# Performance work log

Hardware: AMD Instinct MI355X
Metric: run time of the kernel (lower is better)

The kernel has to match this reference:

```python
import jax, jax.numpy as jnp
import numpy as np

N = 100000       # nodes
E = 3200000      # edges (avg degree 32)
C_IN = 32        # input_channels


def _glorot(key, shape):
    lim = float(np.sqrt(6.0 / (shape[0] + shape[1])))
    return jax.random.uniform(key, shape, jnp.float32, -lim, lim)


def setup_inputs() -> dict:
    key = jax.random.key(0)
    ks = jax.random.split(key, 8)
    x = jax.random.normal(ks[0], (N, C_IN), jnp.float32)
    edge_index = jax.random.randint(ks[1], (2, E), 0, N, dtype=jnp.int64)
    return {
        "x": x,
        "edge_index": edge_index,
        "W1": _glorot(ks[2], (C_IN, 16)), "b1": jnp.zeros((16,), jnp.float32),
        "W2": _glorot(ks[3], (16, 32)),   "b2": jnp.zeros((32,), jnp.float32),
        "W3": _glorot(ks[4], (32, 16)),   "b3": jnp.zeros((16,), jnp.float32),
        "Wfc": _glorot(ks[5], (16, 1)),   "bfc": jnp.zeros((1,), jnp.float32),
    }


def _gcn_conv(x, W, b, src, dst, norm, n):
    # PyG GCNConv: transform then degree-normalized scatter-add (self-loops in src/dst)
    h = x @ W                              # [N, out]
    m = h[src] * norm[:, None]             # gather + per-edge scale
    return jax.ops.segment_sum(m, dst, num_segments=n) + b


def reference(x, edge_index, W1, b1, W2, b2, W3, b3, Wfc, bfc):
    n = x.shape[0]
    loops = jnp.arange(n, dtype=edge_index.dtype)
    src = jnp.concatenate([edge_index[0], loops])   # add self-loops
    dst = jnp.concatenate([edge_index[1], loops])
    deg = jax.ops.segment_sum(jnp.ones(src.shape[0], x.dtype), dst, num_segments=n)
    dis = jnp.where(deg > 0, jax.lax.rsqrt(deg), jnp.zeros((), x.dtype))
    norm = dis[src] * dis[dst]                      # symmetric D^-1/2 A D^-1/2

    h = jax.nn.relu(_gcn_conv(x, W1, b1, src, dst, norm, n))
    h = jax.nn.relu(_gcn_conv(h, W2, b2, src, dst, norm, n))
    h = jax.nn.relu(_gcn_conv(h, W3, b3, src, dst, norm, n))
    out = h @ Wfc + bfc                             # [N, 1]
    return jnp.mean(out)
```

## Files before the change

kernel.cpp:

```cpp
#include <hip/hip_runtime.h>

static constexpr int BLK = 256;
static constexpr int CHUNK = 4096;
static constexpr int BSHIFT = 7;
static constexpr int BNODES = 128;
static constexpr int MAXNB = 1024;

__device__ __forceinline__ float bf_lo(unsigned u) { return __uint_as_float(u << 16); }
__device__ __forceinline__ float bf_hi(unsigned u) { return __uint_as_float(u & 0xFFFF0000u); }
__device__ __forceinline__ unsigned bf_r(float f) {
    unsigned x = __float_as_uint(f);
    x += 0x7fffu + ((x >> 16) & 1u);
    return x >> 16;
}
__device__ __forceinline__ unsigned bf_pack(float lo, float hi) {
    return bf_r(lo) | (bf_r(hi) << 16);
}


__global__ __launch_bounds__(BLK) void k_hist(const int* __restrict__ dst, int* __restrict__ ghist,
                                              int e, int NB, int NBLK) {
    __shared__ int h[MAXNB];
    for (int i = threadIdx.x; i < NB; i += BLK) h[i] = 0;
    __syncthreads();
    int base = blockIdx.x * CHUNK;
    int lim = min(e - base, CHUNK);
    bool v4 = ((((size_t)(dst + base)) & 15) == 0);
    if (v4 && lim == CHUNK) {
        const int4* d4 = (const int4*)(dst + base);
        for (int q = threadIdx.x; q < CHUNK / 4; q += BLK) {
            int4 v = d4[q];
            atomicAdd(&h[v.x >> BSHIFT], 1);
            atomicAdd(&h[v.y >> BSHIFT], 1);
            atomicAdd(&h[v.z >> BSHIFT], 1);
            atomicAdd(&h[v.w >> BSHIFT], 1);
        }
    } else {
        for (int r = threadIdx.x; r < lim; r += BLK) atomicAdd(&h[dst[base + r] >> BSHIFT], 1);
    }
    __syncthreads();
    for (int b = threadIdx.x; b < NB; b += BLK) ghist[b * NBLK + blockIdx.x] = h[b];
}

__global__ void k_scan1(const int* __restrict__ in, int* __restrict__ excl,
                        int* __restrict__ partials, int n) {
    __shared__ int s[BLK];
    int i = blockIdx.x * BLK + threadIdx.x;
    int v = (i < n) ? in[i] : 0;
    s[threadIdx.x] = v;
    __syncthreads();
    for (int off = 1; off < BLK; off <<= 1) {
        int t = ((int)threadIdx.x >= off) ? s[threadIdx.x - off] : 0;
        __syncthreads();
        s[threadIdx.x] += t;
        __syncthreads();
    }
    if (i < n) excl[i] = s[threadIdx.x] - v;
    if (threadIdx.x == BLK - 1) partials[blockIdx.x] = s[BLK - 1];
}

__global__ void k_scan2(int* __restrict__ partials, int P) {
    __shared__ int s[1024];
    int carry = 0;
    for (int base = 0; base < P; base += 1024) {
        int i = base + (int)threadIdx.x;
        int v = (i < P) ? partials[i] : 0;
        s[threadIdx.x] = v;
        __syncthreads();
        for (int off = 1; off < 1024; off <<= 1) {
            int t = ((int)threadIdx.x >= off) ? s[threadIdx.x - off] : 0;
            __syncthreads();
            s[threadIdx.x] += t;
            __syncthreads();
        }
        if (i < P) partials[i] = carry + s[threadIdx.x] - v;
        carry += s[1023];
        __syncthreads();
    }
}

__global__ void k_scan3(int* __restrict__ excl, const int* __restrict__ partials, int n) {
    int i = blockIdx.x * BLK + threadIdx.x;
    if (i < n) excl[i] += partials[blockIdx.x];
}

__global__ __launch_bounds__(BLK) void k_bin(const int* __restrict__ src, const int* __restrict__ dst,
                                             const int* __restrict__ goff, unsigned int* __restrict__ keys,
                                             int e, int NB, int NBLK) {
    __shared__ int hcur[MAXNB];
    __shared__ int sstart[MAXNB + 1];
    __shared__ unsigned int stage[CHUNK];
    __shared__ unsigned short bkt[CHUNK];
    for (int i = threadIdx.x; i < NB; i += BLK) hcur[i] = 0;
    __syncthreads();
    int base = blockIdx.x * CHUNK;
    int lim = min(e - base, CHUNK);
    bool v4 = ((((size_t)(dst + base)) & 15) == 0) && ((((size_t)(src + base)) & 15) == 0) && (lim == CHUNK);
    if (v4) {
        const int4* d4 = (const int4*)(dst + base);
        for (int q = threadIdx.x; q < CHUNK / 4; q += BLK) {
            int4 v = d4[q];
            atomicAdd(&hcur[v.x >> BSHIFT], 1);
            atomicAdd(&hcur[v.y >> BSHIFT], 1);
            atomicAdd(&hcur[v.z >> BSHIFT], 1);
            atomicAdd(&hcur[v.w >> BSHIFT], 1);
        }
    } else {
        for (int r = threadIdx.x; r < lim; r += BLK) atomicAdd(&hcur[dst[base + r] >> BSHIFT], 1);
    }
    __syncthreads();
    for (int i = threadIdx.x; i < MAXNB; i += BLK) sstart[i] = (i < NB) ? hcur[i] : 0;
    __syncthreads();
    for (int off = 1; off < MAXNB; off <<= 1) {
        int tv[MAXNB / BLK];
#pragma unroll
        for (int j = 0; j < MAXNB / BLK; ++j) {
            int i = (int)threadIdx.x + j * BLK;
            tv[j] = (i >= off) ? sstart[i - off] : 0;
        }
        __syncthreads();
#pragma unroll
        for (int j = 0; j < MAXNB / BLK; ++j) sstart[(int)threadIdx.x + j * BLK] += tv[j];
        __syncthreads();
    }
    int ex[MAXNB / BLK];
#pragma unroll
    for (int j = 0; j < MAXNB / BLK; ++j) {
        int i = (int)threadIdx.x + j * BLK;
        ex[j] = sstart[i] - ((i < NB) ? hcur[i] : 0);
    }
    __syncthreads();
#pragma unroll
    for (int j = 0; j < MAXNB / BLK; ++j) {
        int i = (int)threadIdx.x + j * BLK;
        sstart[i] = ex[j];
        if (i < NB) hcur[i] = ex[j];
    }
    __syncthreads();
    if (v4) {
        const int4* s4 = (const int4*)(src + base);
        const int4* d4 = (const int4*)(dst + base);
        for (int q = threadIdx.x; q < CHUNK / 4; q += BLK) {
            int4 sv = s4[q];
            int4 dv = d4[q];
#pragma unroll
            for (int u = 0; u < 4; ++u) {
                int s = (u == 0) ? sv.x : (u == 1) ? sv.y : (u == 2) ? sv.z : sv.w;
                int d = (u == 0) ? dv.x : (u == 1) ? dv.y : (u == 2) ? dv.z : dv.w;
                int b = d >> BSHIFT;
                int pos = atomicAdd(&hcur[b], 1);
                stage[pos] = (unsigned)s | ((unsigned)(d & (BNODES - 1)) << 20);
                bkt[pos] = (unsigned short)b;
            }
        }
    } else {
        for (int r = threadIdx.x; r < lim; r += BLK) {
            int s = src[base + r], d = dst[base + r];
            int b = d >> BSHIFT;
            int pos = atomicAdd(&hcur[b], 1);
            stage[pos] = (unsigned)s | ((unsigned)(d & (BNODES - 1)) << 20);
            bkt[pos] = (unsigned short)b;
        }
    }
    __syncthreads();
    for (int j = threadIdx.x; j < lim; j += BLK) {
        int b = bkt[j];
        keys[goff[b * NBLK + blockIdx.x] + (j - sstart[b])] = stage[j];
    }
}

__global__ __launch_bounds__(BLK) void k_sortb(const unsigned int* __restrict__ keys,
                                               const int* __restrict__ goff,
                                               unsigned int* __restrict__ sorted,
                                               int* __restrict__ node_off, float* __restrict__ dis,
                                               int n, int NB, int NBLK, int e) {
    __shared__ int cnt[BNODES];
    __shared__ int sc[BNODES];
    __shared__ int cur[BNODES];
    int b = blockIdx.x;
    int start = goff[b * NBLK];
    int end = (b + 1 < NB) ? goff[(b + 1) * NBLK] : e;
    if (threadIdx.x < BNODES) cnt[threadIdx.x] = 0;
    __syncthreads();
    int astart = (start + 3) & ~3;
    if (astart > end) astart = end;
    int nq = (end - astart) >> 2;
    for (int k = start + (int)threadIdx.x; k < astart; k += BLK) atomicAdd(&cnt[keys[k] >> 20], 1);
    {
        const uint4* k4 = (const uint4*)(keys + astart);
        for (int q = threadIdx.x; q < nq; q += BLK) {
            uint4 v = k4[q];
            atomicAdd(&cnt[v.x >> 20], 1);
            atomicAdd(&cnt[v.y >> 20], 1);
            atomicAdd(&cnt[v.z >> 20], 1);
            atomicAdd(&cnt[v.w >> 20], 1);
        }
    }
    for (int k = astart + (nq << 2) + (int)threadIdx.x; k < end; k += BLK) atomicAdd(&cnt[keys[k] >> 20], 1);
    __syncthreads();
    if (threadIdx.x < BNODES) sc[threadIdx.x] = cnt[threadIdx.x];
    __syncthreads();
    for (int off = 1; off < BNODES; off <<= 1) {
        int v = ((int)threadIdx.x < BNODES && (int)threadIdx.x >= off) ? sc[threadIdx.x - off] : 0;
        __syncthreads();
        if ((int)threadIdx.x < BNODES) sc[threadIdx.x] += v;
        __syncthreads();
    }
    if ((int)threadIdx.x < BNODES) {
        int excl = sc[threadIdx.x] - cnt[threadIdx.x];
        cur[threadIdx.x] = start + excl;
        int d = b * BNODES + (int)threadIdx.x;
        if (d < n) {
            node_off[d] = start + excl;
            dis[d] = rsqrtf(1.0f + (float)cnt[threadIdx.x]);
        }
    }
    if (b == NB - 1 && threadIdx.x == 0) node_off[n] = e;
    __syncthreads();
    for (int k = start + (int)threadIdx.x; k < astart; k += BLK) {
        unsigned key = keys[k];
        int pos = atomicAdd(&cur[key >> 20], 1);
        sorted[pos] = key & 0xFFFFFu;
    }
    {
        const uint4* k4 = (const uint4*)(keys + astart);
        for (int q = threadIdx.x; q < nq; q += BLK) {
            uint4 v = k4[q];
#pragma unroll
            for (int u = 0; u < 4; ++u) {
                unsigned key = (u == 0) ? v.x : (u == 1) ? v.y : (u == 2) ? v.z : v.w;
                int pos = atomicAdd(&cur[key >> 20], 1);
                sorted[pos] = key & 0xFFFFFu;
            }
        }
    }
    for (int k = astart + (nq << 2) + (int)threadIdx.x; k < end; k += BLK) {
        unsigned key = keys[k];
        int pos = atomicAdd(&cur[key >> 20], 1);
        sorted[pos] = key & 0xFFFFFu;
    }
}


template <int CIN, int COUT, bool BIAS, bool RELU_OUT, bool SCALE_OUT>
__global__ void k_transform(const float* __restrict__ in, const float* __restrict__ W,
                            const float* __restrict__ bias, const float* __restrict__ dis,
                            float* __restrict__ out, int n) {
    int t = blockIdx.x * BLK + threadIdx.x;
    int node = t / COUT, c = t % COUT;
    if (node >= n) return;
    const float* row = in + (size_t)node * CIN;
    float acc = BIAS ? bias[c] : 0.0f;
#pragma unroll
    for (int k = 0; k < CIN; ++k) acc = fmaf(row[k], W[k * COUT + c], acc);
    if (RELU_OUT) acc = fmaxf(acc, 0.0f);
    if (SCALE_OUT) acc *= dis[node];
    out[t] = acc;
}

__global__ void k_transform1_bf(const float* __restrict__ in, const float* __restrict__ W,
                                const float* __restrict__ dis, unsigned* __restrict__ out, int n) {
    int t = blockIdx.x * BLK + threadIdx.x;
    int node = t >> 3, j = t & 7;
    if (node >= n) return;
    const float* row = in + (size_t)node * 32;
    float a0 = 0.0f, a1 = 0.0f;
#pragma unroll
    for (int k = 0; k < 32; ++k) {
        float v = row[k];
        a0 = fmaf(v, W[k * 16 + 2 * j], a0);
        a1 = fmaf(v, W[k * 16 + 2 * j + 1], a1);
    }
    float sd = dis[node];
    out[t] = bf_pack(a0 * sd, a1 * sd);
}

template <int WMODE>
__global__ __launch_bounds__(BLK) void k_agg(const unsigned* __restrict__ in, const float* __restrict__ dis,
                                             const float* __restrict__ bias,
                                             const float* __restrict__ W2, const float* __restrict__ b2,
                                             const float* __restrict__ W3,
                                             const float* __restrict__ Wfc, const float* __restrict__ bfc,
                                             const unsigned int* __restrict__ sorted,
                                             const int* __restrict__ node_off,
                                             void* __restrict__ outv, int n) {
    int t = blockIdx.x * BLK + threadIdx.x;
    int d = t >> 2, j = t & 3;
    bool valid = d < n;
    int dd = valid ? d : 0;
    int k = node_off[dd], end = node_off[dd + 1];
    if (!valid) end = k;
    const uint2* inrow = (const uint2*)in;
    uint2 zz; zz.x = 0u; zz.y = 0u;
    uint2 ws = valid ? inrow[((size_t)dd << 2) + j] : zz;
    float a00 = bf_lo(ws.x), a10 = bf_hi(ws.x), a20 = bf_lo(ws.y), a30 = bf_hi(ws.y);
    float a01 = 0.0f, a11 = 0.0f, a21 = 0.0f, a31 = 0.0f;
    for (; k < end && (k & 3); ++k) {
        uint2 w = inrow[((size_t)sorted[k] << 2) + j];
        a00 += bf_lo(w.x); a10 += bf_hi(w.x); a20 += bf_lo(w.y); a30 += bf_hi(w.y);
    }
    for (; k + 7 < end; k += 8) {
        uint4 i0 = *(const uint4*)(sorted + k);
        uint4 i1 = *(const uint4*)(sorted + k + 4);
        uint2 w0 = inrow[((size_t)i0.x << 2) + j];
        uint2 w1 = inrow[((size_t)i0.y << 2) + j];
        uint2 w2 = inrow[((size_t)i0.z << 2) + j];
        uint2 w3 = inrow[((size_t)i0.w << 2) + j];
        uint2 w4 = inrow[((size_t)i1.x << 2) + j];
        uint2 w5 = inrow[((size_t)i1.y << 2) + j];
        uint2 w6 = inrow[((size_t)i1.z << 2) + j];
        uint2 w7 = inrow[((size_t)i1.w << 2) + j];
        a00 += (bf_lo(w0.x) + bf_lo(w2.x)) + (bf_lo(w4.x) + bf_lo(w6.x));
        a01 += (bf_lo(w1.x) + bf_lo(w3.x)) + (bf_lo(w5.x) + bf_lo(w7.x));
        a10 += (bf_hi(w0.x) + bf_hi(w2.x)) + (bf_hi(w4.x) + bf_hi(w6.x));
        a11 += (bf_hi(w1.x) + bf_hi(w3.x)) + (bf_hi(w5.x) + bf_hi(w7.x));
        a20 += (bf_lo(w0.y) + bf_lo(w2.y)) + (bf_lo(w4.y) + bf_lo(w6.y));
        a21 += (bf_lo(w1.y) + bf_lo(w3.y)) + (bf_lo(w5.y) + bf_lo(w7.y));
        a30 += (bf_hi(w0.y) + bf_hi(w2.y)) + (bf_hi(w4.y) + bf_hi(w6.y));
        a31 += (bf_hi(w1.y) + bf_hi(w3.y)) + (bf_hi(w5.y) + bf_hi(w7.y));
    }
    for (; k < end; ++k) {
        uint2 w = inrow[((size_t)sorted[k] << 2) + j];
        a00 += bf_lo(w.x); a10 += bf_hi(w.x); a20 += bf_lo(w.y); a30 += bf_hi(w.y);
    }
    float sd = dis[dd];
    float a0 = (a00 + a01) * sd;
    float a1 = (a10 + a11) * sd;
    float a2 = (a20 + a21) * sd;
    float a3 = (a30 + a31) * sd;

    if (WMODE == 0) {
        uint2* out = (uint2*)outv;
        if (valid) {
            uint2 r;
            r.x = bf_pack(sd * fmaxf(bias[4 * j] + a0, 0.0f), sd * fmaxf(bias[4 * j + 1] + a1, 0.0f));
            r.y = bf_pack(sd * fmaxf(bias[4 * j + 2] + a2, 0.0f), sd * fmaxf(bias[4 * j + 3] + a3, 0.0f));
            out[((size_t)d << 2) + j] = r;
        }
    } else if (WMODE == 1) {
        float hh[8];
#pragma unroll
        for (int p = 0; p < 8; ++p) hh[p] = b2[j + 4 * p];
#pragma unroll
        for (int kk = 0; kk < 4; ++kk) {
            float r0 = __shfl(a0, kk, 4);
            float r1 = __shfl(a1, kk, 4);
            float r2 = __shfl(a2, kk, 4);
            float r3 = __shfl(a3, kk, 4);
#pragma unroll
            for (int p = 0; p < 8; ++p) {
                int m = j + 4 * p;
                hh[p] = fmaf(r0, W2[(4 * kk) * 32 + m], hh[p]);
                hh[p] = fmaf(r1, W2[(4 * kk + 1) * 32 + m], hh[p]);
                hh[p] = fmaf(r2, W2[(4 * kk + 2) * 32 + m], hh[p]);
                hh[p] = fmaf(r3, W2[(4 * kk + 3) * 32 + m], hh[p]);
            }
        }
#pragma unroll
        for (int p = 0; p < 8; ++p) hh[p] = fmaxf(hh[p], 0.0f);
        float z0 = 0.0f, z1 = 0.0f, z2 = 0.0f, z3 = 0.0f;
#pragma unroll
        for (int kk = 0; kk < 4; ++kk) {
#pragma unroll
            for (int p = 0; p < 8; ++p) {
                float u = __shfl(hh[p], kk, 4);
                int m = kk + 4 * p;
                z0 = fmaf(u, W3[m * 16 + 4 * j], z0);
                z1 = fmaf(u, W3[m * 16 + 4 * j + 1], z1);
                z2 = fmaf(u, W3[m * 16 + 4 * j + 2], z2);
                z3 = fmaf(u, W3[m * 16 + 4 * j + 3], z3);
            }
        }
        uint2* out = (uint2*)outv;
        if (valid) {
            uint2 r;
            r.x = bf_pack(z0 * sd, z1 * sd);
            r.y = bf_pack(z2 * sd, z3 * sd);
            out[((size_t)d << 2) + j] = r;
        }
    } else {
        float* partials = (float*)outv;
        float contrib = 0.0f;
        if (valid) {
            contrib = bfc[0] * 0.25f;
            contrib = fmaf(fmaxf(bias[4 * j] + a0, 0.0f), Wfc[4 * j], contrib);
            contrib = fmaf(fmaxf(bias[4 * j + 1] + a1, 0.0f), Wfc[4 * j + 1], contrib);
            contrib = fmaf(fmaxf(bias[4 * j + 2] + a2, 0.0f), Wfc[4 * j + 2], contrib);
            contrib = fmaf(fmaxf(bias[4 * j + 3] + a3, 0.0f), Wfc[4 * j + 3], contrib);
        }
#pragma unroll
        for (int m = 1; m < 64; m <<= 1) contrib += __shfl_xor(contrib, m, 64);
        __shared__ float sw[BLK / 64];
        if ((threadIdx.x & 63) == 0) sw[threadIdx.x >> 6] = contrib;
        __syncthreads();
        if (threadIdx.x == 0) {
            float tt = 0.0f;
#pragma unroll
            for (int w = 0; w < BLK / 64; ++w) tt += sw[w];
            partials[blockIdx.x] = tt;
        }
    }
}

__global__ __launch_bounds__(BLK) void k_reduce(const float* __restrict__ partials, int P,
                                                float* __restrict__ out, float inv_n) {
    float v = 0.0f;
    for (int i = threadIdx.x; i < P; i += BLK) v += partials[i];
#pragma unroll
    for (int m = 1; m < 64; m <<= 1) v += __shfl_xor(v, m, 64);
    __shared__ float sw[BLK / 64];
    if ((threadIdx.x & 63) == 0) sw[threadIdx.x >> 6] = v;
    __syncthreads();
    if (threadIdx.x == 0) {
        float tt = 0.0f;
#pragma unroll
        for (int w = 0; w < BLK / 64; ++w) tt += sw[w];
        out[0] = tt * inv_n;
    }
}


__global__ void k_deg_init(float* __restrict__ deg, int n) {
    int i = blockIdx.x * BLK + threadIdx.x;
    if (i < n) deg[i] = 1.0f;
}
__global__ void k_deg_count(const int* __restrict__ dst, float* __restrict__ deg, int e) {
    int i = blockIdx.x * BLK + threadIdx.x;
    if (i < e) atomicAdd(&deg[dst[i]], 1.0f);
}
__global__ void k_deg_rsqrt(float* __restrict__ deg, int n) {
    int i = blockIdx.x * BLK + threadIdx.x;
    if (i < n) deg[i] = rsqrtf(deg[i]);
}
template <int C, bool RELU_IN, bool BIAS>
__global__ void k_selfloop(const float* __restrict__ h, const float* __restrict__ dis,
                           const float* __restrict__ b, float* __restrict__ agg, int n) {
    int t = blockIdx.x * BLK + threadIdx.x;
    int node = t / C, c = t % C;
    if (node >= n) return;
    float w = dis[node];
    float v = h[t];
    if (RELU_IN) v = fmaxf(v, 0.0f);
    agg[t] = (BIAS ? b[c] : 0.0f) + v * w * w;
}
template <int C, bool RELU_IN>
__global__ void k_scatter(const int* __restrict__ src, const int* __restrict__ dst,
                          const float* __restrict__ h, const float* __restrict__ dis,
                          float* __restrict__ agg, int e) {
    int t = blockIdx.x * BLK + threadIdx.x;
    int edge = t / C, c = t % C;
    if (edge >= e) return;
    int s = src[edge], d = dst[edge];
    float w = dis[s] * dis[d];
    float v = h[(size_t)s * C + c];
    if (RELU_IN) v = fmaxf(v, 0.0f);
    atomicAdd(&agg[(size_t)d * C + c], v * w);
}
__global__ void k_zero(float* __restrict__ out) { out[0] = 0.0f; }
__global__ void k_final(const float* __restrict__ h, const float* __restrict__ Wfc,
                        const float* __restrict__ bfc, float* __restrict__ out, int n,
                        float inv_n) {
    int i = blockIdx.x * BLK + threadIdx.x;
    float v = 0.0f;
    if (i < n) {
        float acc = bfc[0];
        const float* row = h + (size_t)i * 16;
#pragma unroll
        for (int c = 0; c < 16; ++c) acc = fmaf(fmaxf(row[c], 0.0f), Wfc[c], acc);
        v = acc;
    }
#pragma unroll
    for (int off = 32; off > 0; off >>= 1) v += __shfl_down(v, off);
    __shared__ float sw[BLK / 64];
    int wid = threadIdx.x >> 6;
    if ((threadIdx.x & 63) == 0) sw[wid] = v;
    __syncthreads();
    if (threadIdx.x == 0) {
        float t = 0.0f;
#pragma unroll
        for (int w = 0; w < BLK / 64; ++w) t += sw[w];
        atomicAdd(out, t * inv_n);
    }
}


extern "C" void kernel_launch(void* const* d_in, const int* in_sizes, int n_in,
                              void* d_out, int out_size, void* d_ws, size_t ws_size,
                              hipStream_t stream) {
    const float* x   = (const float*)d_in[0];
    const int* ei    = (const int*)d_in[1];
    const float* W1  = (const float*)d_in[2];
    const float* b1  = (const float*)d_in[3];
    const float* W2  = (const float*)d_in[4];
    const float* b2  = (const float*)d_in[5];
    const float* W3  = (const float*)d_in[6];
    const float* b3  = (const float*)d_in[7];
    const float* Wfc = (const float*)d_in[8];
    const float* bfc = (const float*)d_in[9];
    float* out = (float*)d_out;

    const int n = in_sizes[0] / 32;
    const int e = in_sizes[1] / 2;
    const int* src = ei;
    const int* dst = ei + e;

    auto g1 = [](long long work) { return dim3((unsigned)((work + BLK - 1) / BLK)); };

    const int NB   = (n + BNODES - 1) >> BSHIFT;
    const int NBLK = (e + CHUNK - 1) / CHUNK;
    const long long L = (long long)NB * NBLK;
    const int P = (int)((L + BLK - 1) / BLK);
    const int PM = (int)(((long long)n * 4 + BLK - 1) / BLK);

    auto align_up = [](size_t v) { return (v + 255) & ~(size_t)255; };
    size_t off = 0;
    auto carve = [&](size_t bytes) { size_t o = off; off += align_up(bytes); return o; };
    char* base = (char*)d_ws;
    size_t o_dis   = carve((size_t)n * 4);
    size_t o_noff  = carve(((size_t)n + 1) * 4);
    size_t o_ghist = carve((size_t)L * 4);
    size_t o_goff  = carve((size_t)L * 4);
    size_t o_part  = carve(((size_t)P + 1) * 4);
    size_t o_pm    = carve((size_t)PM * 4);
    size_t o_A     = carve((size_t)n * 16 * 2);
    size_t o_B     = carve((size_t)n * 16 * 2);
    size_t o_keys  = carve((size_t)e * 4);
    size_t o_sort  = carve((size_t)e * 4);
    bool ok = (off <= ws_size) && (NB <= MAXNB) && (n < (1 << 20));

    if (ok) {
        float* dis  = (float*)(base + o_dis);
        int* noff   = (int*)(base + o_noff);
        int* ghist  = (int*)(base + o_ghist);
        int* goff   = (int*)(base + o_goff);
        int* part   = (int*)(base + o_part);
        float* pm   = (float*)(base + o_pm);
        unsigned* A = (unsigned*)(base + o_A);
        unsigned* B = (unsigned*)(base + o_B);
        unsigned int* keys   = (unsigned int*)(base + o_keys);
        unsigned int* sorted = (unsigned int*)(base + o_sort);

        k_hist<<<dim3(NBLK), BLK, 0, stream>>>(dst, ghist, e, NB, NBLK);
        k_scan1<<<g1(L), BLK, 0, stream>>>(ghist, goff, part, (int)L);
        k_scan2<<<1, 1024, 0, stream>>>(part, P);
        k_scan3<<<g1(L), BLK, 0, stream>>>(goff, part, (int)L);
        k_bin<<<dim3(NBLK), BLK, 0, stream>>>(src, dst, goff, keys, e, NB, NBLK);
        k_sortb<<<dim3(NB), BLK, 0, stream>>>(keys, goff, sorted, noff, dis, n, NB, NBLK, e);

        k_transform1_bf<<<g1((long long)n * 8), BLK, 0, stream>>>(x, W1, dis, A, n);
        k_agg<0><<<g1((long long)n * 4), BLK, 0, stream>>>(A, dis, b1, nullptr, nullptr, nullptr, nullptr, nullptr,
                                                           sorted, noff, B, n);
        k_agg<1><<<g1((long long)n * 4), BLK, 0, stream>>>(B, dis, nullptr, W2, b2, W3, nullptr, nullptr,
                                                           sorted, noff, A, n);
        k_agg<2><<<g1((long long)n * 4), BLK, 0, stream>>>(A, dis, b3, nullptr, nullptr, nullptr, Wfc, bfc,
                                                           sorted, noff, pm, n);
        k_reduce<<<1, BLK, 0, stream>>>(pm, PM, out, 1.0f / (float)n);
    } else {
        float* dis = (float*)d_ws;
        float* A = dis + (((size_t)n + 255) & ~(size_t)255);
        float* B = A + (size_t)n * 32;

        k_deg_init<<<g1(n), BLK, 0, stream>>>(dis, n);
        k_deg_count<<<g1(e), BLK, 0, stream>>>(dst, dis, e);
        k_deg_rsqrt<<<g1(n), BLK, 0, stream>>>(dis, n);

        k_transform<32, 16, false, false, false><<<g1((long long)n * 16), BLK, 0, stream>>>(x, W1, nullptr, nullptr, A, n);
        k_selfloop<16, false, true><<<g1((long long)n * 16), BLK, 0, stream>>>(A, dis, b1, B, n);
        k_scatter<16, false><<<g1((long long)e * 16), BLK, 0, stream>>>(src, dst, A, dis, B, e);

        k_selfloop<16, true, false><<<g1((long long)n * 16), BLK, 0, stream>>>(B, dis, nullptr, A, n);
        k_scatter<16, true><<<g1((long long)e * 16), BLK, 0, stream>>>(src, dst, B, dis, A, e);
        k_transform<16, 32, true, true, false><<<g1((long long)n * 32), BLK, 0, stream>>>(A, W2, b2, nullptr, B, n);

        k_transform<32, 16, false, false, false><<<g1((long long)n * 16), BLK, 0, stream>>>(B, W3, nullptr, nullptr, A, n);
        k_selfloop<16, false, true><<<g1((long long)n * 16), BLK, 0, stream>>>(A, dis, b3, B, n);
        k_scatter<16, false><<<g1((long long)e * 16), BLK, 0, stream>>>(src, dst, A, dis, B, e);

        k_zero<<<1, 1, 0, stream>>>(out);
        k_final<<<g1(n), BLK, 0, stream>>>(B, Wfc, bfc, out, n, 1.0f / (float)n);
    }
}
```

Baseline: 186.9 us.

## Split each node's neighbor aggregation across four thread groups with shuffle reduction

Each node's aggregation now uses 16 threads instead of 4. Four groups of 4 lanes take interleaved 8-edge chunks of the neighbor list, and their partial sums are combined with xor shuffles. The aim is more memory-level parallelism and shorter per-thread loops for the latency-bound gather over about 32 neighbors per node. In exchange it launches four times as many threads, duplicates the epilogue math (W2/W3 transform) across groups, and adds shuffle overhead.

```diff
diff --git a/kernel.cpp b/kernel.cpp
--- a/kernel.cpp
+++ b/kernel.cpp
@@ -285,21 +285,30 @@
                                              const int* __restrict__ node_off,
                                              void* __restrict__ outv, int n) {
     int t = blockIdx.x * BLK + threadIdx.x;
-    int d = t >> 2, j = t & 3;
+    int d = t >> 4;
+    int j = t & 3;
+    int g = (t >> 2) & 3;
     bool valid = d < n;
     int dd = valid ? d : 0;
-    int k = node_off[dd], end = node_off[dd + 1];
-    if (!valid) end = k;
+    int start = node_off[dd], end = node_off[dd + 1];
+    if (!valid) end = start;
     const uint2* inrow = (const uint2*)in;
-    uint2 zz; zz.x = 0u; zz.y = 0u;
-    uint2 ws = valid ? inrow[((size_t)dd << 2) + j] : zz;
-    float a00 = bf_lo(ws.x), a10 = bf_hi(ws.x), a20 = bf_lo(ws.y), a30 = bf_hi(ws.y);
+    float a00 = 0.0f, a10 = 0.0f, a20 = 0.0f, a30 = 0.0f;
     float a01 = 0.0f, a11 = 0.0f, a21 = 0.0f, a31 = 0.0f;
-    for (; k < end && (k & 3); ++k) {
-        uint2 w = inrow[((size_t)sorted[k] << 2) + j];
-        a00 += bf_lo(w.x); a10 += bf_hi(w.x); a20 += bf_lo(w.y); a30 += bf_hi(w.y);
-    }
-    for (; k + 7 < end; k += 8) {
+    if (g == 0 && valid) {
+        uint2 ws = inrow[((size_t)dd << 2) + j];
+        a00 = bf_lo(ws.x); a10 = bf_hi(ws.x); a20 = bf_lo(ws.y); a30 = bf_hi(ws.y);
+    }
+    int astart = (start + 3) & ~3;
+    if (astart > end) astart = end;
+    if (g == 0) {
+        for (int k = start; k < astart; ++k) {
+            uint2 w = inrow[((size_t)sorted[k] << 2) + j];
+            a00 += bf_lo(w.x); a10 += bf_hi(w.x); a20 += bf_lo(w.y); a30 += bf_hi(w.y);
+        }
+    }
+    int nful = (end - astart) >> 3;
+    for (int k = astart + g * 8; k + 7 < end; k += 32) {
         uint4 i0 = *(const uint4*)(sorted + k);
         uint4 i1 = *(const uint4*)(sorted + k + 4);
         uint2 w0 = inrow[((size_t)i0.x << 2) + j];
@@ -319,19 +328,29 @@
         a30 += (bf_hi(w0.y) + bf_hi(w2.y)) + (bf_hi(w4.y) + bf_hi(w6.y));
         a31 += (bf_hi(w1.y) + bf_hi(w3.y)) + (bf_hi(w5.y) + bf_hi(w7.y));
     }
-    for (; k < end; ++k) {
-        uint2 w = inrow[((size_t)sorted[k] << 2) + j];
-        a00 += bf_lo(w.x); a10 += bf_hi(w.x); a20 += bf_lo(w.y); a30 += bf_hi(w.y);
+    if (g == (nful & 3)) {
+        for (int k = astart + (nful << 3); k < end; ++k) {
+            uint2 w = inrow[((size_t)sorted[k] << 2) + j];
+            a00 += bf_lo(w.x); a10 += bf_hi(w.x); a20 += bf_lo(w.y); a30 += bf_hi(w.y);
+        }
+    }
+    float s0 = a00 + a01, s1 = a10 + a11, s2 = a20 + a21, s3 = a30 + a31;
+#pragma unroll
+    for (int m = 4; m < 16; m <<= 1) {
+        s0 += __shfl_xor(s0, m, 16);
+        s1 += __shfl_xor(s1, m, 16);
+        s2 += __shfl_xor(s2, m, 16);
+        s3 += __shfl_xor(s3, m, 16);
     }
     float sd = dis[dd];
-    float a0 = (a00 + a01) * sd;
-    float a1 = (a10 + a11) * sd;
-    float a2 = (a20 + a21) * sd;
-    float a3 = (a30 + a31) * sd;
+    float a0 = s0 * sd;
+    float a1 = s1 * sd;
+    float a2 = s2 * sd;
+    float a3 = s3 * sd;
 
     if (WMODE == 0) {
         uint2* out = (uint2*)outv;
-        if (valid) {
+        if (valid && g == 0) {
             uint2 r;
             r.x = bf_pack(sd * fmaxf(bias[4 * j] + a0, 0.0f), sd * fmaxf(bias[4 * j + 1] + a1, 0.0f));
             r.y = bf_pack(sd * fmaxf(bias[4 * j + 2] + a2, 0.0f), sd * fmaxf(bias[4 * j + 3] + a3, 0.0f));
@@ -372,7 +391,7 @@
             }
         }
         uint2* out = (uint2*)outv;
-        if (valid) {
+        if (valid && g == 0) {
             uint2 r;
             r.x = bf_pack(z0 * sd, z1 * sd);
             r.y = bf_pack(z2 * sd, z3 * sd);
@@ -381,7 +400,7 @@
     } else {
         float* partials = (float*)outv;
         float contrib = 0.0f;
-        if (valid) {
+        if (valid && g == 0) {
             contrib = bfc[0] * 0.25f;
             contrib = fmaf(fmaxf(bias[4 * j] + a0, 0.0f), Wfc[4 * j], contrib);
             contrib = fmaf(fmaxf(bias[4 * j + 1] + a1, 0.0f), Wfc[4 * j + 1], contrib);
@@ -510,7 +529,7 @@
     const int NBLK = (e + CHUNK - 1) / CHUNK;
     const long long L = (long long)NB * NBLK;
     const int P = (int)((L + BLK - 1) / BLK);
-    const int PM = (int)(((long long)n * 4 + BLK - 1) / BLK);
+    const int PM = (int)(((long long)n * 16 + BLK - 1) / BLK);
 
     auto align_up = [](size_t v) { return (v + 255) & ~(size_t)255; };
     size_t off = 0;
@@ -548,12 +567,12 @@
         k_sortb<<<dim3(NB), BLK, 0, stream>>>(keys, goff, sorted, noff, dis, n, NB, NBLK, e);
 
         k_transform1_bf<<<g1((long long)n * 8), BLK, 0, stream>>>(x, W1, dis, A, n);
-        k_agg<0><<<g1((long long)n * 4), BLK, 0, stream>>>(A, dis, b1, nullptr, nullptr, nullptr, nullptr, nullptr,
-                                                           sorted, noff, B, n);
-        k_agg<1><<<g1((long long)n * 4), BLK, 0, stream>>>(B, dis, nullptr, W2, b2, W3, nullptr, nullptr,
-                                                           sorted, noff, A, n);
-        k_agg<2><<<g1((long long)n * 4), BLK, 0, stream>>>(A, dis, b3, nullptr, nullptr, nullptr, Wfc, bfc,
-                                                           sorted, noff, pm, n);
+        k_agg<0><<<g1((long long)n * 16), BLK, 0, stream>>>(A, dis, b1, nullptr, nullptr, nullptr, nullptr, nullptr,
+                                                            sorted, noff, B, n);
+        k_agg<1><<<g1((long long)n * 16), BLK, 0, stream>>>(B, dis, nullptr, W2, b2, W3, nullptr, nullptr,
+                                                            sorted, noff, A, n);
+        k_agg<2><<<g1((long long)n * 16), BLK, 0, stream>>>(A, dis, b3, nullptr, nullptr, nullptr, Wfc, bfc,
+                                                            sorted, noff, pm, n);
         k_reduce<<<1, BLK, 0, stream>>>(pm, PM, out, 1.0f / (float)n);
     } else {
         float* dis = (float*)d_ws;
```

After: 231.4 us. 23.8% more time.
